# Kernel tuning notes

Hardware: AMD Instinct MI355X
Metric: run time of the kernel (lower is better)

## Reference

```python
import jax, jax.numpy as jnp
import numpy as np

N = 100000        # num nodes
F_IN = 256        # params['topo_feature']
C = 128           # params['num_edge'] (hidden & GCN channels)
E = 1_600_000     # num edges (avg degree 16)


def setup_inputs() -> dict:
    key = jax.random.key(0)
    k = jax.random.split(key, 6)
    x = jax.random.normal(k[0], (N, F_IN), dtype=jnp.float32)
    edge_index = jax.random.randint(k[1], (2, E), 0, N, dtype=jnp.int32)
    # fc1: Linear(F_IN, C)
    W1 = jax.random.normal(k[2], (C, F_IN), dtype=jnp.float32) * (1.0 / np.sqrt(F_IN))
    b1 = jnp.zeros((C,), dtype=jnp.float32)
    # GCNConv linear: Linear(C, C, bias=False) weight + separate bias added post-aggregation
    W2 = jax.random.normal(k[3], (C, C), dtype=jnp.float32) * (1.0 / np.sqrt(C))
    b2 = jnp.zeros((C,), dtype=jnp.float32)
    return {"x": x, "edge_index": edge_index, "W1": W1, "b1": b1, "W2": W2, "b2": b2}


def reference(x, edge_index, W1, b1, W2, b2):
    # fc1 + relu
    h = jax.nn.relu(x @ W1.T + b1)                       # [N, C]
    # GCNConv: transform, add self-loops, sym-normalize, scatter-add
    z = h @ W2.T                                         # [N, C]
    loop = jnp.arange(N, dtype=edge_index.dtype)
    src = jnp.concatenate([edge_index[0], loop])         # [E+N]
    dst = jnp.concatenate([edge_index[1], loop])         # [E+N]
    deg = jax.ops.segment_sum(jnp.ones_like(dst, jnp.float32), dst, num_segments=N)
    dinv = jnp.where(deg > 0, jax.lax.rsqrt(jnp.maximum(deg, 1.0)), 0.0)
    norm = (dinv[src] * dinv[dst])[:, None]              # [E+N, 1]
    out = jax.ops.segment_sum(z[src] * norm, dst, num_segments=N) + b2
    return out
```

## Files before the change

### kernel.cpp

```cpp
#include <hip/hip_runtime.h>

typedef unsigned short ushort;
typedef __bf16 bf16x8 __attribute__((ext_vector_type(8)));
typedef float f32x4 __attribute__((ext_vector_type(4)));

#define F_IN 256
#define CCH  128
#define BSH  7
#define BNODES 128
#define NBUCK 1024
#define CHUNK 2048

#define LDA 40
#define LDH 136

__device__ __forceinline__ ushort f2bf(float f) {
    union { float f; unsigned i; } u; u.f = f;
    unsigned r = u.i + 0x7fffu + ((u.i >> 16) & 1u);
    return (ushort)(r >> 16);
}
__device__ __forceinline__ float2 bf2f2(unsigned u) {
    union { unsigned i; float f; } lo, hi;
    lo.i = u << 16;
    hi.i = u & 0xffff0000u;
    return make_float2(lo.f, hi.f);
}

__global__ __launch_bounds__(256)
void hist_cvt(const int* __restrict__ dst, int* __restrict__ histC, int* __restrict__ histT,
              int E, int nchunks, int ncp,
              const float* __restrict__ W1, const float* __restrict__ W2,
              ushort* __restrict__ w1b, ushort* __restrict__ w2b)
{
    const int blk = blockIdx.x, t = threadIdx.x;
    if (blk >= nchunks) {
        int i = (blk - nchunks) * 256 + t;
        if (i < CCH * F_IN) w1b[i] = f2bf(W1[i]);
        else {
            int j = i - CCH * F_IN;
            if (j < CCH * CCH) w2b[j] = f2bf(W2[j]);
        }
        return;
    }
    __shared__ int h[NBUCK];
    for (int i = t; i < NBUCK; i += 256) h[i] = 0;
    __syncthreads();
    int cb = blk * CHUNK, ce = min(cb + CHUNK, E);
    for (int e = cb + t; e < ce; e += 256)
        atomicAdd(&h[dst[e] >> BSH], 1);
    __syncthreads();
    for (int i = t; i < NBUCK; i += 256) {
        int v = h[i];
        histC[blk * NBUCK + i] = v;
        histT[i * ncp + blk]   = v;
    }
}

__global__ __launch_bounds__(256)
void scan_buckets(const int* __restrict__ histT, int* __restrict__ prefT,
                  int* __restrict__ btot, int nchunks, int ncp)
{
    const int b = blockIdx.x * 4 + (threadIdx.x >> 6);
    const int lane = threadIdx.x & 63;
    int carry = 0;
    for (int c = 0; c < nchunks; c += 64) {
        int idx = c + lane;
        int v = (idx < nchunks) ? histT[b * ncp + idx] : 0;
        int inc = v;
#pragma unroll
        for (int off = 1; off < 64; off <<= 1) {
            int x = __shfl_up(inc, off, 64);
            if (lane >= off) inc += x;
        }
        if (idx < nchunks) prefT[b * ncp + idx] = carry + inc - v;
        carry += __shfl(inc, 63, 64);
    }
    if (lane == 0) btot[b] = carry;
}

__global__ __launch_bounds__(256)
void partition_kernel(const int* __restrict__ src, const int* __restrict__ dst,
                      const int* __restrict__ histC, const int* __restrict__ prefT,
                      const int* __restrict__ btot, int* __restrict__ gbase,
                      unsigned* __restrict__ pairs, int E, int ncp)
{
    __shared__ int lbase[NBUCK];
    __shared__ int lcur[NBUCK];
    __shared__ int rb2[NBUCK];
    __shared__ int base_s[NBUCK];
    __shared__ int ssum[256];
    __shared__ unsigned sp[CHUNK];
    __shared__ ushort  sb[CHUNK];
    const int t = threadIdx.x, blk = blockIdx.x;

    int4 cv = *(const int4*)&histC[blk * NBUCK + 4 * t];
    int tsum = cv.x + cv.y + cv.z + cv.w;
    ssum[t] = tsum;
    __syncthreads();
    for (int off = 1; off < 256; off <<= 1) {
        int x = (t >= off) ? ssum[t - off] : 0;
        __syncthreads();
        ssum[t] += x;
        __syncthreads();
    }
    int texcl = ssum[t] - tsum;
    lbase[4 * t]     = texcl;
    lbase[4 * t + 1] = texcl + cv.x;
    lbase[4 * t + 2] = texcl + cv.x + cv.y;
    lbase[4 * t + 3] = texcl + cv.x + cv.y + cv.z;
    lcur[4 * t]     = lbase[4 * t];
    lcur[4 * t + 1] = lbase[4 * t + 1];
    lcur[4 * t + 2] = lbase[4 * t + 2];
    lcur[4 * t + 3] = lbase[4 * t + 3];
    __syncthreads();

    int4 bt = *(const int4*)&btot[4 * t];
    int bsum = bt.x + bt.y + bt.z + bt.w;
    ssum[t] = bsum;
    __syncthreads();
    for (int off = 1; off < 256; off <<= 1) {
        int x = (t >= off) ? ssum[t - off] : 0;
        __syncthreads();
        ssum[t] += x;
        __syncthreads();
    }
    int bexcl = ssum[t] - bsum;
    base_s[4 * t]     = bexcl;
    base_s[4 * t + 1] = bexcl + bt.x;
    base_s[4 * t + 2] = bexcl + bt.x + bt.y;
    base_s[4 * t + 3] = bexcl + bt.x + bt.y + bt.z;
    if (blk == 0) {
        *(int4*)&gbase[4 * t] = *(int4*)&base_s[4 * t];
        if (t == 255) gbase[NBUCK] = ssum[255];
    }
    __syncthreads();
    for (int i = t; i < NBUCK; i += 256)
        rb2[i] = base_s[i] + prefT[i * ncp + blk];
    __syncthreads();

    const int cb = blk * CHUNK, ce = min(cb + CHUNK, E);
    for (int e = cb + t; e < ce; e += 256) {
        int d = dst[e];
        int b = d >> BSH;
        unsigned packed = ((unsigned)src[e] << BSH) | (unsigned)(d & (BNODES - 1));
        int p = atomicAdd(&lcur[b], 1);
        sp[p] = packed;
        sb[p] = (ushort)b;
    }
    __syncthreads();
    const int cnt = ce - cb;
    for (int i = t; i < cnt; i += 256) {
        int b = sb[i];
        pairs[rb2[b] + (i - lbase[b])] = sp[i];
    }
}

__global__ __launch_bounds__(256)
void bucket_csr(const unsigned* __restrict__ pairs, const int* __restrict__ base,
                int* __restrict__ row_start, float* __restrict__ dinv,
                unsigned* __restrict__ csr, int N, int E)
{
    __shared__ int deg[BNODES];
    __shared__ int s[BNODES];
    __shared__ int cur[BNODES];
    const int b = blockIdx.x, t = threadIdx.x;
    if (t < BNODES) deg[t] = 0;
    __syncthreads();
    const int rb = base[b], re = base[b + 1];
    for (int e = rb + t; e < re; e += 256)
        atomicAdd(&deg[pairs[e] & (BNODES - 1)], 1);
    __syncthreads();
    int v = (t < BNODES) ? deg[t] : 0;
    if (t < BNODES) s[t] = v;
    __syncthreads();
    for (int off = 1; off < BNODES; off <<= 1) {
        int x = (t >= off && t < BNODES) ? s[t - off] : 0;
        __syncthreads();
        if (t < BNODES) s[t] += x;
        __syncthreads();
    }
    const int n0 = b << BSH;
    if (t < BNODES) {
        int excl = s[t] - v;
        cur[t] = excl;
        if (n0 + t < N) {
            row_start[n0 + t] = rb + excl;
            dinv[n0 + t] = rsqrtf((float)v + 1.0f);
        }
    }
    if (b == gridDim.x - 1 && t == 0) row_start[N] = E;
    __syncthreads();
    for (int e = rb + t; e < re; e += 256) {
        unsigned p = pairs[e];
        int l = p & (BNODES - 1);
        int slot = atomicAdd(&cur[l], 1);
        csr[rb + slot] = p >> BSH;
    }
}

__global__ __launch_bounds__(256)
void gemm_fused(const float* __restrict__ X, const ushort* __restrict__ W1b,
                const ushort* __restrict__ W2b, const float* __restrict__ b1,
                const float* __restrict__ dinv, ushort* __restrict__ Zq, int M)
{
    __shared__ ushort smem[22528];
    ushort* Ht  = smem;
    ushort* BsB = smem + 17408;
    const int tid = threadIdx.x;
    const int wave = tid >> 6, lane = tid & 63;
    const int wm = (wave & 1) * 64, wn = (wave >> 1) * 64;
    const int lr = lane & 15, lq = lane >> 4;
    const int m0 = blockIdx.x * 128;

    const int ldr  = tid >> 2;
    const int ldkq = (tid & 3) * 8;

    f32x4 acc[4][4] = {};
    float4 ar[2][2];
    uint4  br[2];
    {
#pragma unroll
        for (int it = 0; it < 2; it++) {
            int row = ldr + it * 64;
            ar[it][0] = make_float4(0.f, 0.f, 0.f, 0.f);
            ar[it][1] = make_float4(0.f, 0.f, 0.f, 0.f);
            if (m0 + row < M) {
                ar[it][0] = *(const float4*)&X[(long)(m0 + row) * F_IN + ldkq];
                ar[it][1] = *(const float4*)&X[(long)(m0 + row) * F_IN + ldkq + 4];
            }
            br[it] = *(const uint4*)&W1b[(long)row * F_IN + ldkq];
        }
    }
    for (int k0 = 0; k0 < F_IN; k0 += 32) {
        ushort* As = smem + (k0 & 32) * 320;
        ushort* Bs = As + 5120;
#pragma unroll
        for (int it = 0; it < 2; it++) {
            int row = ldr + it * 64;
            ushort u[8] = { f2bf(ar[it][0].x), f2bf(ar[it][0].y), f2bf(ar[it][0].z), f2bf(ar[it][0].w),
                            f2bf(ar[it][1].x), f2bf(ar[it][1].y), f2bf(ar[it][1].z), f2bf(ar[it][1].w) };
            *(uint4*)&As[row * LDA + ldkq] = *(uint4*)u;
            *(uint4*)&Bs[row * LDA + ldkq] = br[it];
        }
        __syncthreads();
        if (k0 + 32 < F_IN) {
            int kn = k0 + 32;
#pragma unroll
            for (int it = 0; it < 2; it++) {
                int row = ldr + it * 64;
                ar[it][0] = make_float4(0.f, 0.f, 0.f, 0.f);
                ar[it][1] = make_float4(0.f, 0.f, 0.f, 0.f);
                if (m0 + row < M) {
                    ar[it][0] = *(const float4*)&X[(long)(m0 + row) * F_IN + kn + ldkq];
                    ar[it][1] = *(const float4*)&X[(long)(m0 + row) * F_IN + kn + ldkq + 4];
                }
                br[it] = *(const uint4*)&W1b[(long)row * F_IN + kn + ldkq];
            }
        }
        bf16x8 af[4], bfr[4];
#pragma unroll
        for (int t4 = 0; t4 < 4; t4++) {
            af[t4]  = *(bf16x8*)&As[(wm + t4 * 16 + lr) * LDA + lq * 8];
            bfr[t4] = *(bf16x8*)&Bs[(wn + t4 * 16 + lr) * LDA + lq * 8];
        }
#pragma unroll
        for (int i = 0; i < 4; i++)
#pragma unroll
            for (int j = 0; j < 4; j++)
                acc[i][j] = __builtin_amdgcn_mfma_f32_16x16x32_bf16(af[i], bfr[j], acc[i][j], 0, 0, 0);
    }
    __syncthreads();

    {
        float bv[4];
#pragma unroll
        for (int j = 0; j < 4; j++) bv[j] = b1[wn + j * 16 + lr];
#pragma unroll
        for (int i = 0; i < 4; i++)
#pragma unroll
            for (int r = 0; r < 4; r++) {
                int row = wm + i * 16 + lq * 4 + r;
#pragma unroll
                for (int j = 0; j < 4; j++)
                    Ht[row * LDH + wn + j * 16 + lr] = f2bf(fmaxf(acc[i][j][r] + bv[j], 0.f));
            }
    }
    __syncthreads();

    f32x4 acc2[4][4] = {};
    {
#pragma unroll
        for (int it = 0; it < 2; it++)
            br[it] = *(const uint4*)&W2b[(long)(ldr + it * 64) * CCH + ldkq];
    }
    for (int k0 = 0; k0 < CCH; k0 += 32) {
#pragma unroll
        for (int it = 0; it < 2; it++)
            *(uint4*)&BsB[(ldr + it * 64) * LDA + ldkq] = br[it];
        __syncthreads();
        if (k0 + 32 < CCH) {
#pragma unroll
            for (int it = 0; it < 2; it++)
                br[it] = *(const uint4*)&W2b[(long)(ldr + it * 64) * CCH + k0 + 32 + ldkq];
        }
        bf16x8 af[4], bfr[4];
#pragma unroll
        for (int t4 = 0; t4 < 4; t4++) {
            af[t4]  = *(bf16x8*)&Ht[(wm + t4 * 16 + lr) * LDH + k0 + lq * 8];
            bfr[t4] = *(bf16x8*)&BsB[(wn + t4 * 16 + lr) * LDA + lq * 8];
        }
#pragma unroll
        for (int i = 0; i < 4; i++)
#pragma unroll
            for (int j = 0; j < 4; j++)
                acc2[i][j] = __builtin_amdgcn_mfma_f32_16x16x32_bf16(af[i], bfr[j], acc2[i][j], 0, 0, 0);
        __syncthreads();
    }

#pragma unroll
    for (int i = 0; i < 4; i++)
#pragma unroll
        for (int r = 0; r < 4; r++) {
            int row = wm + i * 16 + lq * 4 + r;
            float di = (m0 + row < M) ? dinv[m0 + row] : 0.f;
#pragma unroll
            for (int j = 0; j < 4; j++)
                Ht[row * LDH + wn + j * 16 + lr] = f2bf(acc2[i][j][r] * di);
        }
    __syncthreads();
    {
        int colq = tid & 15, row0 = tid >> 4;
#pragma unroll
        for (int i = 0; i < 8; i++) {
            int row = row0 + i * 16;
            if (m0 + row < M)
                *(uint4*)&Zq[(long)(m0 + row) * CCH + colq * 8] =
                    *(uint4*)&Ht[row * LDH + colq * 8];
        }
    }
}

__global__ __launch_bounds__(256)
void gather_nodes(const unsigned* __restrict__ zq, const unsigned* __restrict__ csr,
                  const int* __restrict__ row_start, const float* __restrict__ dinv,
                  const float* __restrict__ b2, float* __restrict__ out, int N)
{
    const int node = blockIdx.x * 4 + (threadIdx.x >> 6);
    const int lane = threadIdx.x & 63;
    if (node >= N) return;

    float2 zs = bf2f2(zq[(long)node * 64 + lane]);
    float acc0 = zs.x, acc1 = zs.y;

    const int rs = row_start[node];
    const int re = row_start[node + 1];
    int j = rs;
    for (; j + 8 <= re; j += 8) {
        unsigned sI[8], zv[8];
#pragma unroll
        for (int q = 0; q < 8; q++) sI[q] = csr[j + q];
#pragma unroll
        for (int q = 0; q < 8; q++) zv[q] = zq[(long)sI[q] * 64 + lane];
#pragma unroll
        for (int q = 0; q < 8; q++) { float2 f = bf2f2(zv[q]); acc0 += f.x; acc1 += f.y; }
    }
    for (; j < re; j++) {
        float2 f = bf2f2(zq[(long)csr[j] * 64 + lane]);
        acc0 += f.x; acc1 += f.y;
    }

    float di = dinv[node];
    float2 o;
    o.x = b2[lane * 2 + 0] + di * acc0;
    o.y = b2[lane * 2 + 1] + di * acc1;
    *(float2*)&out[(long)node * CCH + lane * 2] = o;
}

extern "C" void kernel_launch(void* const* d_in, const int* in_sizes, int n_in,
                              void* d_out, int out_size, void* d_ws, size_t ws_size,
                              hipStream_t stream)
{
    const float* x  = (const float*)d_in[0];
    const int*   ei = (const int*)d_in[1];
    const float* W1 = (const float*)d_in[2];
    const float* b1 = (const float*)d_in[3];
    const float* W2 = (const float*)d_in[4];
    const float* b2 = (const float*)d_in[5];
    float* out = (float*)d_out;

    const int N = in_sizes[0] / F_IN;
    const int E = in_sizes[1] / 2;
    const int* src = ei;
    const int* dst = ei + E;

    const int nchunks = (E + CHUNK - 1) / CHUNK;
    const int ncp     = (nchunks + 63) & ~63;
    const int nbuck   = (N + BNODES - 1) / BNODES;
    const int ngrid   = (N + 127) / 128;
    const int ncvt    = (CCH * F_IN + CCH * CCH + 255) / 256;

    char* ws = (char*)d_ws;
    ushort* zq    = (ushort*)ws;   ws += (size_t)N * CCH * 2;
    ushort* w1b   = (ushort*)ws;   ws += (size_t)CCH * F_IN * 2;
    ushort* w2b   = (ushort*)ws;   ws += (size_t)CCH * CCH * 2;
    unsigned* prs = (unsigned*)ws; ws += (size_t)E * 4;
    unsigned* csr = (unsigned*)ws; ws += (size_t)E * 4;
    int* rstart   = (int*)ws;      ws += ((size_t)N + 1) * 4;
    float* dinv   = (float*)ws;    ws += (size_t)N * 4;
    int* histC    = (int*)ws;      ws += (size_t)nchunks * NBUCK * 4;
    int* histT    = (int*)ws;      ws += (size_t)NBUCK * ncp * 4;
    int* prefT    = (int*)ws;      ws += (size_t)NBUCK * ncp * 4;
    int* btot     = (int*)ws;      ws += NBUCK * 4;
    int* gbase    = (int*)ws;      ws += (NBUCK + 1) * 4;

    hist_cvt<<<nchunks + ncvt, 256, 0, stream>>>(dst, histC, histT, E, nchunks, ncp, W1, W2, w1b, w2b);
    scan_buckets<<<NBUCK / 4, 256, 0, stream>>>(histT, prefT, btot, nchunks, ncp);
    partition_kernel<<<nchunks, 256, 0, stream>>>(src, dst, histC, prefT, btot, gbase, prs, E, ncp);
    bucket_csr<<<nbuck, 256, 0, stream>>>(prs, gbase, rstart, dinv, csr, N, E);

    gemm_fused<<<ngrid, 256, 0, stream>>>(x, w1b, w2b, b1, dinv, zq, N);

    gather_nodes<<<(N + 3) / 4, 256, 0, stream>>>((const unsigned*)zq, csr, rstart, dinv, b2, out, N);
}
```

Before: 339.4 us.

## Restructure fused GEMM with direct-to-LDS W1 loads, XOR swizzle, register-resident W2

The fused fc1/GCN-linear GEMM now uses XOR-swizzled unpadded LDS layouts in place of padded strides, and streams W1 tiles straight into LDS with global_load_lds. W1 is pre-swizzled during the bf16 conversion to match. The k-loop double-buffers A and B with a single barrier per iteration, and the second GEMM reads W2 fragments directly from global into registers with prefetch instead of staging them through LDS. The smaller LDS footprint and a launch-bounds hint of 4 blocks per CU aim for higher occupancy and fewer barriers. The costs are more register pressure and reliance on the swizzle staying consistent between the conversion kernel and the GEMM.

```diff
diff --git a/kernel.cpp b/kernel.cpp
--- a/kernel.cpp
+++ b/kernel.cpp
@@ -11,9 +11,6 @@
 #define NBUCK 1024
 #define CHUNK 2048
 
-#define LDA 40
-#define LDH 136
-
 __device__ __forceinline__ ushort f2bf(float f) {
     union { float f; unsigned i; } u; u.f = f;
     unsigned r = u.i + 0x7fffu + ((u.i >> 16) & 1u);
@@ -25,6 +22,10 @@
     hi.i = u & 0xffff0000u;
     return make_float2(lo.f, hi.f);
 }
+__device__ __forceinline__ void gload_lds16(const void* g, void* l) {
+    __builtin_amdgcn_global_load_lds((const __attribute__((address_space(1))) unsigned*)g,
+                                     (__attribute__((address_space(3))) unsigned*)l, 16, 0, 0);
+}
 
 __global__ __launch_bounds__(256)
 void hist_cvt(const int* __restrict__ dst, int* __restrict__ histC, int* __restrict__ histT,
@@ -35,8 +36,11 @@
     const int blk = blockIdx.x, t = threadIdx.x;
     if (blk >= nchunks) {
         int i = (blk - nchunks) * 256 + t;
-        if (i < CCH * F_IN) w1b[i] = f2bf(W1[i]);
-        else {
+        if (i < CCH * F_IN) {
+            int c  = i & 31;
+            int cs = c ^ (((i >> 9) & 3) << 3);
+            w1b[(i & ~31) | cs] = f2bf(W1[i]);
+        } else {
             int j = i - CCH * F_IN;
             if (j < CCH * CCH) w2b[j] = f2bf(W2[j]);
         }
@@ -198,78 +202,89 @@
     }
 }
 
-__global__ __launch_bounds__(256)
+__global__ __launch_bounds__(256, 4)
 void gemm_fused(const float* __restrict__ X, const ushort* __restrict__ W1b,
                 const ushort* __restrict__ W2b, const float* __restrict__ b1,
                 const float* __restrict__ dinv, ushort* __restrict__ Zq, int M)
 {
-    __shared__ ushort smem[22528];
-    ushort* Ht  = smem;
-    ushort* BsB = smem + 17408;
-    const int tid = threadIdx.x;
+    __shared__ ushort smem[16384];
+    ushort* Ht = smem;
+    const int tid  = threadIdx.x;
     const int wave = tid >> 6, lane = tid & 63;
     const int wm = (wave & 1) * 64, wn = (wave >> 1) * 64;
     const int lr = lane & 15, lq = lane >> 4;
     const int m0 = blockIdx.x * 128;
 
-    const int ldr  = tid >> 2;
-    const int ldkq = (tid & 3) * 8;
-
-    f32x4 acc[4][4] = {};
+    const int arow = tid >> 2;
+    const int aq   = tid & 3;
+
     float4 ar[2][2];
-    uint4  br[2];
-    {
+    auto loadX = [&](int k0) {
 #pragma unroll
         for (int it = 0; it < 2; it++) {
-            int row = ldr + it * 64;
+            int row = arow + it * 64;
             ar[it][0] = make_float4(0.f, 0.f, 0.f, 0.f);
             ar[it][1] = make_float4(0.f, 0.f, 0.f, 0.f);
             if (m0 + row < M) {
-                ar[it][0] = *(const float4*)&X[(long)(m0 + row) * F_IN + ldkq];
-                ar[it][1] = *(const float4*)&X[(long)(m0 + row) * F_IN + ldkq + 4];
+                const float* p = &X[(long)(m0 + row) * F_IN + k0 + aq * 8];
+                ar[it][0] = *(const float4*)p;
+                ar[it][1] = *(const float4*)(p + 4);
             }
-            br[it] = *(const uint4*)&W1b[(long)row * F_IN + ldkq];
-        }
-    }
-    for (int k0 = 0; k0 < F_IN; k0 += 32) {
-        ushort* As = smem + (k0 & 32) * 320;
-        ushort* Bs = As + 5120;
+        }
+    };
+    auto writeA = [&](ushort* As) {
 #pragma unroll
         for (int it = 0; it < 2; it++) {
-            int row = ldr + it * 64;
+            int row = arow + it * 64;
             ushort u[8] = { f2bf(ar[it][0].x), f2bf(ar[it][0].y), f2bf(ar[it][0].z), f2bf(ar[it][0].w),
                             f2bf(ar[it][1].x), f2bf(ar[it][1].y), f2bf(ar[it][1].z), f2bf(ar[it][1].w) };
-            *(uint4*)&As[row * LDA + ldkq] = *(uint4*)u;
-            *(uint4*)&Bs[row * LDA + ldkq] = br[it];
-        }
-        __syncthreads();
-        if (k0 + 32 < F_IN) {
-            int kn = k0 + 32;
-#pragma unroll
-            for (int it = 0; it < 2; it++) {
-                int row = ldr + it * 64;
-                ar[it][0] = make_float4(0.f, 0.f, 0.f, 0.f);
-                ar[it][1] = make_float4(0.f, 0.f, 0.f, 0.f);
-                if (m0 + row < M) {
-                    ar[it][0] = *(const float4*)&X[(long)(m0 + row) * F_IN + kn + ldkq];
-                    ar[it][1] = *(const float4*)&X[(long)(m0 + row) * F_IN + kn + ldkq + 4];
-                }
-                br[it] = *(const uint4*)&W1b[(long)row * F_IN + kn + ldkq];
-            }
+            *(uint4*)&As[row * 32 + ((aq ^ ((row >> 1) & 3)) << 3)] = *(uint4*)u;
+        }
+    };
+    auto stageB = [&](int k0, ushort* Bs) {
+#pragma unroll
+        for (int it = 0; it < 2; it++) {
+            int r0 = wave * 32 + it * 16;
+            const ushort* g = &W1b[(long)(r0 + (lane >> 2)) * F_IN + k0 + (lane & 3) * 8];
+            gload_lds16(g, &Bs[r0 * 32]);
+        }
+    };
+
+    f32x4 acc[4][4] = {};
+    loadX(0);
+    stageB(0, smem + 4096);
+    writeA(smem);
+    __syncthreads();
+    for (int k0 = 0; k0 < F_IN; k0 += 32) {
+        const int cur = (k0 >> 5) & 1;
+        ushort* As = smem + cur * 8192;
+        ushort* Bs = As + 4096;
+        const bool more = (k0 + 32 < F_IN);
+        if (more) {
+            stageB(k0 + 32, smem + (cur ^ 1) * 8192 + 4096);
+            loadX(k0 + 32);
         }
         bf16x8 af[4], bfr[4];
 #pragma unroll
         for (int t4 = 0; t4 < 4; t4++) {
-            af[t4]  = *(bf16x8*)&As[(wm + t4 * 16 + lr) * LDA + lq * 8];
-            bfr[t4] = *(bf16x8*)&Bs[(wn + t4 * 16 + lr) * LDA + lq * 8];
+            int ra = wm + t4 * 16 + lr;
+            int rb = wn + t4 * 16 + lr;
+            af[t4]  = *(bf16x8*)&As[ra * 32 + ((lq ^ ((ra >> 1) & 3)) << 3)];
+            bfr[t4] = *(bf16x8*)&Bs[rb * 32 + ((lq ^ ((rb >> 1) & 3)) << 3)];
         }
 #pragma unroll
         for (int i = 0; i < 4; i++)
 #pragma unroll
             for (int j = 0; j < 4; j++)
                 acc[i][j] = __builtin_amdgcn_mfma_f32_16x16x32_bf16(af[i], bfr[j], acc[i][j], 0, 0, 0);
-    }
-    __syncthreads();
+        if (more) writeA(smem + (cur ^ 1) * 8192);
+        __syncthreads();
+    }
+
+    uint4 wb[2][4];
+#pragma unroll
+    for (int t4 = 0; t4 < 4; t4++)
+        wb[0][t4] = *(const uint4*)&W2b[(long)(wn + t4 * 16 + lr) * CCH + lq * 8];
 
     {
         float bv[4];
@@ -280,52 +295,49 @@
 #pragma unroll
             for (int r = 0; r < 4; r++) {
                 int row = wm + i * 16 + lq * 4 + r;
+                int rx  = (row & 7) << 3;
 #pragma unroll
                 for (int j = 0; j < 4; j++)
-                    Ht[row * LDH + wn + j * 16 + lr] = f2bf(fmaxf(acc[i][j][r] + bv[j], 0.f));
+                    Ht[row * 128 + ((wn + j * 16 + lr) ^ rx)] = f2bf(fmaxf(acc[i][j][r] + bv[j], 0.f));
             }
     }
     __syncthreads();
 
     f32x4 acc2[4][4] = {};
-    {
-#pragma unroll
-        for (int it = 0; it < 2; it++)
-            br[it] = *(const uint4*)&W2b[(long)(ldr + it * 64) * CCH + ldkq];
-    }
-    for (int k0 = 0; k0 < CCH; k0 += 32) {
-#pragma unroll
-        for (int it = 0; it < 2; it++)
-            *(uint4*)&BsB[(ldr + it * 64) * LDA + ldkq] = br[it];
-        __syncthreads();
-        if (k0 + 32 < CCH) {
-#pragma unroll
-            for (int it = 0; it < 2; it++)
-                br[it] = *(const uint4*)&W2b[(long)(ldr + it * 64) * CCH + k0 + 32 + ldkq];
-        }
-        bf16x8 af[4], bfr[4];
+#pragma unroll
+    for (int kk = 0; kk < 4; kk++) {
+        const int k0 = kk * 32;
+        if (kk < 3) {
+#pragma unroll
+            for (int t4 = 0; t4 < 4; t4++)
+                wb[(kk + 1) & 1][t4] =
+                    *(const uint4*)&W2b[(long)(wn + t4 * 16 + lr) * CCH + k0 + 32 + lq * 8];
+        }
+        bf16x8 af[4];
 #pragma unroll
         for (int t4 = 0; t4 < 4; t4++) {
-            af[t4]  = *(bf16x8*)&Ht[(wm + t4 * 16 + lr) * LDH + k0 + lq * 8];
-            bfr[t4] = *(bf16x8*)&BsB[(wn + t4 * 16 + lr) * LDA + lq * 8];
+            int ra = wm + t4 * 16 + lr;
+            af[t4] = *(bf16x8*)&Ht[ra * 128 + ((k0 + lq * 8) ^ ((ra & 7) << 3))];
         }
 #pragma unroll
         for (int i = 0; i < 4; i++)
 #pragma unroll
             for (int j = 0; j < 4; j++)
-                acc2[i][j] = __builtin_amdgcn_mfma_f32_16x16x32_bf16(af[i], bfr[j], acc2[i][j], 0, 0, 0);
-        __syncthreads();
-    }
+                acc2[i][j] = __builtin_amdgcn_mfma_f32_16x16x32_bf16(af[i], *(bf16x8*)&wb[kk & 1][j],
+                                                                     acc2[i][j], 0, 0, 0);
+    }
+    __syncthreads();
 
 #pragma unroll
     for (int i = 0; i < 4; i++)
 #pragma unroll
         for (int r = 0; r < 4; r++) {
             int row = wm + i * 16 + lq * 4 + r;
+            int rx  = (row & 7) << 3;
             float di = (m0 + row < M) ? dinv[m0 + row] : 0.f;
 #pragma unroll
             for (int j = 0; j < 4; j++)
-                Ht[row * LDH + wn + j * 16 + lr] = f2bf(acc2[i][j][r] * di);
+                Ht[row * 128 + ((wn + j * 16 + lr) ^ rx)] = f2bf(acc2[i][j][r] * di);
         }
     __syncthreads();
     {
@@ -335,7 +347,7 @@
             int row = row0 + i * 16;
             if (m0 + row < M)
                 *(uint4*)&Zq[(long)(m0 + row) * CCH + colq * 8] =
-                    *(uint4*)&Ht[row * LDH + colq * 8];
+                    *(uint4*)&Ht[row * 128 + ((colq * 8) ^ ((row & 7) << 3))];
         }
     }
 }
```

After: 364.8 us. +7.5%, slower.
